# Kernel optimization log

Measured on AMD Instinct MI355X. Metric: run time of the kernel, lower is better.

The kernel has to match this reference:

```python
import jax, jax.numpy as jnp
import numpy as np

LATENT = 32
GRID = 32
G1 = GRID + 1  # 33 samples per axis (align_corners grid)
HID = 128
N_POINTS = 1048576


def _trilinear_sample(emb, points):
    """Faithful F.grid_sample(mode='bilinear', padding_mode='zeros', align_corners=True).
    emb: [(G1)^3, C] flat table; points: [n,3] in [-1,1], (x,y,z) -> (W,H,D)."""
    C = emb.shape[1]
    # torch .view(1, C, D, H, W) on the flat [(G1)^3 * C] buffer: same reshape here.
    vol = emb.reshape(C, G1, G1, G1).transpose(1, 2, 3, 0)  # [D, H, W, C]
    # align_corners=True: u in [-1,1] -> pixel coord (u+1)/2 * (size-1)
    coords = (points + 1.0) * (0.5 * (G1 - 1))
    x, y, z = coords[:, 0], coords[:, 1], coords[:, 2]
    x0 = jnp.floor(x); y0 = jnp.floor(y); z0 = jnp.floor(z)
    fx = x - x0; fy = y - y0; fz = z - z0
    x0i = x0.astype(jnp.int32); y0i = y0.astype(jnp.int32); z0i = z0.astype(jnp.int32)
    x1i = x0i + 1; y1i = y0i + 1; z1i = z0i + 1

    def corner(zi, yi, xi, w):
        valid = ((zi >= 0) & (zi < G1) & (yi >= 0) & (yi < G1)
                 & (xi >= 0) & (xi < G1))
        zc = jnp.clip(zi, 0, G1 - 1)
        yc = jnp.clip(yi, 0, G1 - 1)
        xc = jnp.clip(xi, 0, G1 - 1)
        v = vol[zc, yc, xc]  # [n, C] gather
        return v * (w * valid.astype(w.dtype))[:, None]

    wx0, wx1 = 1.0 - fx, fx
    wy0, wy1 = 1.0 - fy, fy
    wz0, wz1 = 1.0 - fz, fz
    lat = (corner(z0i, y0i, x0i, wz0 * wy0 * wx0)
           + corner(z0i, y0i, x1i, wz0 * wy0 * wx1)
           + corner(z0i, y1i, x0i, wz0 * wy1 * wx0)
           + corner(z0i, y1i, x1i, wz0 * wy1 * wx1)
           + corner(z1i, y0i, x0i, wz1 * wy0 * wx0)
           + corner(z1i, y0i, x1i, wz1 * wy0 * wx1)
           + corner(z1i, y1i, x0i, wz1 * wy1 * wx0)
           + corner(z1i, y1i, x1i, wz1 * wy1 * wx1))
    return lat  # [n, C]


def setup_inputs() -> dict:
    key = jax.random.key(0)
    ks = jax.random.split(key, 8)
    points = jax.random.uniform(ks[0], (N_POINTS, 3), dtype=jnp.float32)  # in [0,1) subset of [-1,1]
    emb = jax.random.normal(ks[1], (G1 ** 3, LATENT), dtype=jnp.float32)
    w1 = jax.random.normal(ks[2], (LATENT, HID), dtype=jnp.float32) * 0.05
    b1 = jax.random.normal(ks[3], (HID,), dtype=jnp.float32) * 0.05
    w2 = jax.random.normal(ks[4], (HID, HID), dtype=jnp.float32) * 0.05
    b2 = jax.random.normal(ks[5], (HID,), dtype=jnp.float32) * 0.05
    w3 = jax.random.normal(ks[6], (HID, 1), dtype=jnp.float32) * 0.05
    b3 = jax.random.normal(ks[7], (1,), dtype=jnp.float32) * 0.05
    return {"points": points, "emb": emb, "w1": w1, "b1": b1,
            "w2": w2, "b2": b2, "w3": w3, "b3": b3}


def reference(points, emb, w1, b1, w2, b2, w3, b3):
    lat = _trilinear_sample(emb, points)                # [n, latent]
    h = jax.nn.relu(lat @ w1 + b1)                      # [n, hid]
    h = jax.nn.relu(h @ w2 + b2)                        # [n, hid]
    sdf = jnp.tanh(h @ w3 + b3)                         # [n, 1]
    return sdf
```

## Files before the change

### kernel.cpp

```cpp
#include <hip/hip_runtime.h>
#include <hip/hip_bf16.h>

#define NPTS 1048576
#define G1I  33
#define NV   35937
#define NC   32
#define HIDD 128

typedef _Float16 h8  __attribute__((ext_vector_type(8)));
typedef _Float16 h4  __attribute__((ext_vector_type(4)));
typedef __fp16   p2  __attribute__((ext_vector_type(2)));
typedef float    f4  __attribute__((ext_vector_type(4)));

#define AS_GLOBAL(p) ((const __attribute__((address_space(1))) char*)(p))
#define AS_LDS(p)    ((__attribute__((address_space(3))) char*)(p))

#define WS_A1  0
#define WS_A2  8192
#define WS_A3  40960
#define WS_EMB 65536
#define WS_NEED (WS_EMB + NV*NC*2)


__global__ __launch_bounds__(256) void vox_prep(
    const float* __restrict__ emb, const float* __restrict__ w1,
    const float* __restrict__ w2, const float* __restrict__ w3,
    char* __restrict__ ws)
{
    __shared__ _Float16 tile[256][NC];
    const int b = blockIdx.x, t = threadIdx.x;
    _Float16* embh = (_Float16*)(ws + WS_EMB);
    if (b < 141) {
        const int v = b*256 + t;
        #pragma unroll
        for (int c = 0; c < NC; ++c) {
            float val = (v < NV) ? emb[c*NV + v] : 0.f;
            const int pos = ((c & 12) << 1) | (c & 3) | ((c >> 4) << 2);
            tile[t][pos] = (_Float16)val;
        }
        __syncthreads();
        if (v < NV) {
            uint4* dst = (uint4*)(embh + v*NC);
            const uint4* src = (const uint4*)&tile[t][0];
            #pragma unroll
            for (int j = 0; j < 4; ++j) dst[j] = src[j];
        }
    } else if (b < 149) {
        const int t2 = b - 141;
        const int ks = t >> 6, l = t & 63;
        const int gq = l >> 4, colh = l & 15;
        _Float16* a2f = (_Float16*)(ws + WS_A2);
        h8 fr;
        #pragma unroll
        for (int i = 0; i < 8; ++i) {
            const int k = 32*ks + 16*(i>>2) + 4*gq + (i&3);
            fr[i] = (_Float16)w2[k*HIDD + 16*t2 + colh];
        }
        *(h8*)(a2f + ((t2*4+ks)*64 + l)*8) = fr;
    } else if (b == 149) {
        _Float16* a1f = (_Float16*)(ws + WS_A1);
        #pragma unroll
        for (int it = 0; it < 2; ++it) {
            const int item = t + it*256;
            const int t8 = item >> 6, l = item & 63;
            const int gq = l >> 4, colh = l & 15;
            h8 fr;
            #pragma unroll
            for (int i = 0; i < 8; ++i) {
                const int k = 16*(i>>2) + 4*gq + (i&3);
                fr[i] = (_Float16)w1[k*HIDD + 16*t8 + colh];
            }
            *(h8*)(a1f + (t8*64 + l)*8) = fr;
        }
    } else {
        _Float16* a3f = (_Float16*)(ws + WS_A3);
        const int j = t >> 6, l = t & 63;
        const int gq = l >> 4;
        h8 fr;
        #pragma unroll
        for (int i = 0; i < 8; ++i) {
            const int k = 32*j + 16*(i>>2) + 4*gq + (i&3);
            fr[i] = (_Float16)w3[k];
        }
        *(h8*)(a3f + (j*64 + l)*8) = fr;
    }
}

__global__ __launch_bounds__(256) void vox_main(
    const float* __restrict__ points, const char* __restrict__ ws,
    const float* __restrict__ b1, const float* __restrict__ b2,
    const float* __restrict__ b3v, float* __restrict__ out)
{
    __shared__ uint4 a2l[2048];

    const int tid  = threadIdx.x;
    const int lane = tid & 63;
    const int wv   = tid >> 6;
    const int gq   = lane >> 4;
    const int colh = lane & 15;

    {
        const uint4* a2g = (const uint4*)(ws + WS_A2);
        #pragma unroll
        for (int j = 0; j < 8; ++j) {
            const uint4* gsrc = a2g + (j*256 + wv*64 + lane);
            uint4*       ldst = ((uint4*)a2l) + (j*256 + wv*64);
            __builtin_amdgcn_global_load_lds(
                (const __attribute__((address_space(1))) void*)AS_GLOBAL(gsrc),
                (__attribute__((address_space(3))) void*)AS_LDS(ldst),
                16, 0, 0);
        }
    }

    const char* embB = (const char*)(ws + WS_EMB);
    const int p = blockIdx.x*256 + tid;
    const float px = points[3*p+0], py = points[3*p+1], pz = points[3*p+2];
    const float xc = (px + 1.f)*16.f, yc = (py + 1.f)*16.f, zc = (pz + 1.f)*16.f;
    const float xf = floorf(xc), yf = floorf(yc), zf = floorf(zc);
    const float fx = xc - xf, fy = yc - yf, fz = zc - zf;
    const int vb = (((int)zf)*G1I + (int)yf)*G1I + (int)xf;

    const h8* a1g = (const h8*)(ws + WS_A1);
    h8 a1fr[8];
    #pragma unroll
    for (int t8 = 0; t8 < 8; ++t8) a1fr[t8] = a1g[t8*64 + lane];

    h8 B2f[4][4];
    #pragma unroll
    for (int pt = 0; pt < 4; ++pt) {
        const int s = pt*16 + colh;
        const float fxs = __shfl(fx, s);
        const float fys = __shfl(fy, s);
        const float fzs = __shfl(fz, s);
        const int   vbs = __shfl(vb, s);
        const char* bz0 = embB + (size_t)((unsigned)vbs*64u + (unsigned)gq*16u);
        const char* bz1 = bz0 + 69696;
        const h8 v0 = *(const h8*)(bz0 +    0);
        const h8 v1 = *(const h8*)(bz0 +   64);
        const h8 v2 = *(const h8*)(bz0 + 2112);
        const h8 v3 = *(const h8*)(bz0 + 2176);
        const h8 v4 = *(const h8*)(bz1 +    0);
        const h8 v5 = *(const h8*)(bz1 +   64);
        const h8 v6 = *(const h8*)(bz1 + 2112);
        const h8 v7 = *(const h8*)(bz1 + 2176);
        const float wx1 = fxs, wx0 = 1.f - fxs;
        const float wy1 = fys, wy0 = 1.f - fys;
        const float wz1 = fzs, wz0 = 1.f - fzs;
        h8 a = (h8){0,0,0,0,0,0,0,0};
        {
            const _Float16 w0 = (_Float16)(wz0*wy0*wx0); const h8 W0 = {w0,w0,w0,w0,w0,w0,w0,w0}; a += W0*v0;
            const _Float16 w1_ = (_Float16)(wz0*wy0*wx1); const h8 W1 = {w1_,w1_,w1_,w1_,w1_,w1_,w1_,w1_}; a += W1*v1;
            const _Float16 w2_ = (_Float16)(wz0*wy1*wx0); const h8 W2 = {w2_,w2_,w2_,w2_,w2_,w2_,w2_,w2_}; a += W2*v2;
            const _Float16 w3_ = (_Float16)(wz0*wy1*wx1); const h8 W3 = {w3_,w3_,w3_,w3_,w3_,w3_,w3_,w3_}; a += W3*v3;
            const _Float16 w4_ = (_Float16)(wz1*wy0*wx0); const h8 W4 = {w4_,w4_,w4_,w4_,w4_,w4_,w4_,w4_}; a += W4*v4;
            const _Float16 w5_ = (_Float16)(wz1*wy0*wx1); const h8 W5 = {w5_,w5_,w5_,w5_,w5_,w5_,w5_,w5_}; a += W5*v5;
            const _Float16 w6_ = (_Float16)(wz1*wy1*wx0); const h8 W6 = {w6_,w6_,w6_,w6_,w6_,w6_,w6_,w6_}; a += W6*v6;
            const _Float16 w7_ = (_Float16)(wz1*wy1*wx1); const h8 W7 = {w7_,w7_,w7_,w7_,w7_,w7_,w7_,w7_}; a += W7*v7;
        }
        f4 acc1[8];
        #pragma unroll
        for (int t8 = 0; t8 < 8; ++t8) acc1[t8] = *(const f4*)(b1 + 16*t8 + 4*gq);
        #pragma unroll
        for (int t8 = 0; t8 < 8; ++t8)
            acc1[t8] = __builtin_amdgcn_mfma_f32_16x16x32_f16(a1fr[t8], a, acc1[t8], 0, 0, 0);
        #pragma unroll
        for (int ks = 0; ks < 4; ++ks) {
            union { h8 v; p2 h[4]; } u;
            const p2 z = {(__fp16)0, (__fp16)0};
            u.h[0] = __builtin_elementwise_max(__builtin_amdgcn_cvt_pkrtz(acc1[2*ks  ][0], acc1[2*ks  ][1]), z);
            u.h[1] = __builtin_elementwise_max(__builtin_amdgcn_cvt_pkrtz(acc1[2*ks  ][2], acc1[2*ks  ][3]), z);
            u.h[2] = __builtin_elementwise_max(__builtin_amdgcn_cvt_pkrtz(acc1[2*ks+1][0], acc1[2*ks+1][1]), z);
            u.h[3] = __builtin_elementwise_max(__builtin_amdgcn_cvt_pkrtz(acc1[2*ks+1][2], acc1[2*ks+1][3]), z);
            B2f[pt][ks] = u.v;
        }
    }

    asm volatile("s_waitcnt vmcnt(0)" ::: "memory");
    __syncthreads();

    const h8* a3g = (const h8*)(ws + WS_A3);
    f4 acc3[4];
    #pragma unroll
    for (int pt = 0; pt < 4; ++pt) acc3[pt] = (f4){0.f,0.f,0.f,0.f};
    #pragma unroll
    for (int q2 = 0; q2 < 4; ++q2) {
        const f4 b2e = *(const f4*)(b2 + 16*(2*q2  ) + 4*gq);
        const f4 b2o = *(const f4*)(b2 + 16*(2*q2+1) + 4*gq);
        f4 acc2e[4], acc2o[4];
        #pragma unroll
        for (int pt = 0; pt < 4; ++pt) { acc2e[pt] = b2e; acc2o[pt] = b2o; }
        #pragma unroll
        for (int ks = 0; ks < 4; ++ks) {
            const h8 fe = *(const h8*)&a2l[((2*q2  )*4 + ks)*64 + lane];
            #pragma unroll
            for (int pt = 0; pt < 4; ++pt)
                acc2e[pt] = __builtin_amdgcn_mfma_f32_16x16x32_f16(fe, B2f[pt][ks], acc2e[pt], 0, 0, 0);
        }
        #pragma unroll
        for (int ks = 0; ks < 4; ++ks) {
            const h8 fo = *(const h8*)&a2l[((2*q2+1)*4 + ks)*64 + lane];
            #pragma unroll
            for (int pt = 0; pt < 4; ++pt)
                acc2o[pt] = __builtin_amdgcn_mfma_f32_16x16x32_f16(fo, B2f[pt][ks], acc2o[pt], 0, 0, 0);
        }
        const h8 a3fr = a3g[q2*64 + lane];
        #pragma unroll
        for (int pt = 0; pt < 4; ++pt) {
            union { h8 v; p2 h[4]; } u;
            const p2 z = {(__fp16)0, (__fp16)0};
            u.h[0] = __builtin_elementwise_max(__builtin_amdgcn_cvt_pkrtz(acc2e[pt][0], acc2e[pt][1]), z);
            u.h[1] = __builtin_elementwise_max(__builtin_amdgcn_cvt_pkrtz(acc2e[pt][2], acc2e[pt][3]), z);
            u.h[2] = __builtin_elementwise_max(__builtin_amdgcn_cvt_pkrtz(acc2o[pt][0], acc2o[pt][1]), z);
            u.h[3] = __builtin_elementwise_max(__builtin_amdgcn_cvt_pkrtz(acc2o[pt][2], acc2o[pt][3]), z);
            acc3[pt] = __builtin_amdgcn_mfma_f32_16x16x32_f16(a3fr, u.v, acc3[pt], 0, 0, 0);
        }
    }

    float sv = 0.f;
    #pragma unroll
    for (int pt = 0; pt < 4; ++pt) if (gq == pt) sv = acc3[pt][0];
    const float zi = sv + b3v[0];
    const float e  = __expf(2.f*zi);
    out[blockIdx.x*256 + tid] = (e - 1.f) / (e + 1.f);
}

extern "C" void kernel_launch(void* const* d_in, const int* in_sizes, int n_in,
                              void* d_out, int out_size, void* d_ws, size_t ws_size,
                              hipStream_t stream)
{
    const float* points = (const float*)d_in[0];
    const float* emb    = (const float*)d_in[1];
    const float* w1     = (const float*)d_in[2];
    const float* b1     = (const float*)d_in[3];
    const float* w2     = (const float*)d_in[4];
    const float* b2     = (const float*)d_in[5];
    const float* w3     = (const float*)d_in[6];
    const float* b3     = (const float*)d_in[7];
    float* out = (float*)d_out;
    char*  ws  = (char*)d_ws;
    if (ws_size < (size_t)WS_NEED) return;

    hipLaunchKernelGGL(vox_prep, dim3(151), dim3(256), 0, stream, emb, w1, w2, w3, ws);
    hipLaunchKernelGGL(vox_main, dim3(NPTS/256), dim3(256), 0, stream,
                       points, ws, b1, b2, b3, out);
}
```

Measured before the change: 144.1 us.

## Gather corner features per 4-lane group then redistribute via ds_bpermute

```diff
diff --git a/kernel.cpp b/kernel.cpp
--- a/kernel.cpp
+++ b/kernel.cpp
@@ -8,7 +8,6 @@
 #define HIDD 128
 
 typedef _Float16 h8  __attribute__((ext_vector_type(8)));
-typedef _Float16 h4  __attribute__((ext_vector_type(4)));
 typedef __fp16   p2  __attribute__((ext_vector_type(2)));
 typedef float    f4  __attribute__((ext_vector_type(4)));
 
@@ -98,6 +97,8 @@
     const int wv   = tid >> 6;
     const int gq   = lane >> 4;
     const int colh = lane & 15;
+    const int q    = lane >> 2;
+    const int ch   = lane & 3;
 
     {
         const uint4* a2g = (const uint4*)(ws + WS_A2);
@@ -113,27 +114,24 @@
     }
 
     const char* embB = (const char*)(ws + WS_EMB);
-    const int p = blockIdx.x*256 + tid;
-    const float px = points[3*p+0], py = points[3*p+1], pz = points[3*p+2];
-    const float xc = (px + 1.f)*16.f, yc = (py + 1.f)*16.f, zc = (pz + 1.f)*16.f;
-    const float xf = floorf(xc), yf = floorf(yc), zf = floorf(zc);
-    const float fx = xc - xf, fy = yc - yf, fz = zc - zf;
-    const int vb = (((int)zf)*G1I + (int)yf)*G1I + (int)xf;
-
-    const h8* a1g = (const h8*)(ws + WS_A1);
-    h8 a1fr[8];
-    #pragma unroll
-    for (int t8 = 0; t8 < 8; ++t8) a1fr[t8] = a1g[t8*64 + lane];
-
-    h8 B2f[4][4];
-    #pragma unroll
-    for (int pt = 0; pt < 4; ++pt) {
-        const int s = pt*16 + colh;
-        const float fxs = __shfl(fx, s);
-        const float fys = __shfl(fy, s);
-        const float fzs = __shfl(fz, s);
-        const int   vbs = __shfl(vb, s);
-        const char* bz0 = embB + (size_t)((unsigned)vbs*64u + (unsigned)gq*16u);
+    const int sgbase = blockIdx.x*256 + wv*64 + q;
+    float px4[4], py4[4], pz4[4];
+    #pragma unroll
+    for (int sh = 0; sh < 4; ++sh) {
+        const float* pp = points + 3*(sgbase + sh*16);
+        px4[sh] = pp[0]; py4[sh] = pp[1]; pz4[sh] = pp[2];
+    }
+
+    h8 accch[4];
+    #pragma unroll
+    for (int sh = 0; sh < 4; ++sh) {
+        const float xc = (px4[sh] + 1.f)*16.f;
+        const float yc = (py4[sh] + 1.f)*16.f;
+        const float zc = (pz4[sh] + 1.f)*16.f;
+        const float xf = floorf(xc), yf = floorf(yc), zf = floorf(zc);
+        const float fxs = xc - xf, fys = yc - yf, fzs = zc - zf;
+        const int vbs = (((int)zf)*G1I + (int)yf)*G1I + (int)xf;
+        const char* bz0 = embB + (size_t)((unsigned)vbs*64u + (unsigned)ch*16u);
         const char* bz1 = bz0 + 69696;
         const h8 v0 = *(const h8*)(bz0 +    0);
         const h8 v1 = *(const h8*)(bz0 +   64);
@@ -147,30 +145,44 @@
         const float wy1 = fys, wy0 = 1.f - fys;
         const float wz1 = fzs, wz0 = 1.f - fzs;
         h8 a = (h8){0,0,0,0,0,0,0,0};
-        {
-            const _Float16 w0 = (_Float16)(wz0*wy0*wx0); const h8 W0 = {w0,w0,w0,w0,w0,w0,w0,w0}; a += W0*v0;
-            const _Float16 w1_ = (_Float16)(wz0*wy0*wx1); const h8 W1 = {w1_,w1_,w1_,w1_,w1_,w1_,w1_,w1_}; a += W1*v1;
-            const _Float16 w2_ = (_Float16)(wz0*wy1*wx0); const h8 W2 = {w2_,w2_,w2_,w2_,w2_,w2_,w2_,w2_}; a += W2*v2;
-            const _Float16 w3_ = (_Float16)(wz0*wy1*wx1); const h8 W3 = {w3_,w3_,w3_,w3_,w3_,w3_,w3_,w3_}; a += W3*v3;
-            const _Float16 w4_ = (_Float16)(wz1*wy0*wx0); const h8 W4 = {w4_,w4_,w4_,w4_,w4_,w4_,w4_,w4_}; a += W4*v4;
-            const _Float16 w5_ = (_Float16)(wz1*wy0*wx1); const h8 W5 = {w5_,w5_,w5_,w5_,w5_,w5_,w5_,w5_}; a += W5*v5;
-            const _Float16 w6_ = (_Float16)(wz1*wy1*wx0); const h8 W6 = {w6_,w6_,w6_,w6_,w6_,w6_,w6_,w6_}; a += W6*v6;
-            const _Float16 w7_ = (_Float16)(wz1*wy1*wx1); const h8 W7 = {w7_,w7_,w7_,w7_,w7_,w7_,w7_,w7_}; a += W7*v7;
-        }
-        f4 acc1[8];
-        #pragma unroll
-        for (int t8 = 0; t8 < 8; ++t8) acc1[t8] = *(const f4*)(b1 + 16*t8 + 4*gq);
-        #pragma unroll
-        for (int t8 = 0; t8 < 8; ++t8)
-            acc1[t8] = __builtin_amdgcn_mfma_f32_16x16x32_f16(a1fr[t8], a, acc1[t8], 0, 0, 0);
+        { const _Float16 w = (_Float16)(wz0*wy0*wx0); const h8 W={w,w,w,w,w,w,w,w}; a += W*v0; }
+        { const _Float16 w = (_Float16)(wz0*wy0*wx1); const h8 W={w,w,w,w,w,w,w,w}; a += W*v1; }
+        { const _Float16 w = (_Float16)(wz0*wy1*wx0); const h8 W={w,w,w,w,w,w,w,w}; a += W*v2; }
+        { const _Float16 w = (_Float16)(wz0*wy1*wx1); const h8 W={w,w,w,w,w,w,w,w}; a += W*v3; }
+        { const _Float16 w = (_Float16)(wz1*wy0*wx0); const h8 W={w,w,w,w,w,w,w,w}; a += W*v4; }
+        { const _Float16 w = (_Float16)(wz1*wy0*wx1); const h8 W={w,w,w,w,w,w,w,w}; a += W*v5; }
+        { const _Float16 w = (_Float16)(wz1*wy1*wx0); const h8 W={w,w,w,w,w,w,w,w}; a += W*v6; }
+        { const _Float16 w = (_Float16)(wz1*wy1*wx1); const h8 W={w,w,w,w,w,w,w,w}; a += W*v7; }
+        accch[sh] = a;
+    }
+
+    const h8* a1g = (const h8*)(ws + WS_A1);
+    h8 a1fr[8];
+    #pragma unroll
+    for (int t8 = 0; t8 < 8; ++t8) a1fr[t8] = a1g[t8*64 + lane];
+
+    const int baddr = 16*colh + 4*gq;
+    h8 B2f[4][4];
+    #pragma unroll
+    for (int pt = 0; pt < 4; ++pt) {
+        union { h8 v; int d[4]; } su, bu;
+        su.v = accch[pt];
+        #pragma unroll
+        for (int j = 0; j < 4; ++j)
+            bu.d[j] = __builtin_amdgcn_ds_bpermute(baddr, su.d[j]);
+        const h8 bf = bu.v;
         #pragma unroll
         for (int ks = 0; ks < 4; ++ks) {
+            f4 ae = *(const f4*)(b1 + 16*(2*ks  ) + 4*gq);
+            f4 ao = *(const f4*)(b1 + 16*(2*ks+1) + 4*gq);
+            ae = __builtin_amdgcn_mfma_f32_16x16x32_f16(a1fr[2*ks  ], bf, ae, 0, 0, 0);
+            ao = __builtin_amdgcn_mfma_f32_16x16x32_f16(a1fr[2*ks+1], bf, ao, 0, 0, 0);
             union { h8 v; p2 h[4]; } u;
             const p2 z = {(__fp16)0, (__fp16)0};
-            u.h[0] = __builtin_elementwise_max(__builtin_amdgcn_cvt_pkrtz(acc1[2*ks  ][0], acc1[2*ks  ][1]), z);
-            u.h[1] = __builtin_elementwise_max(__builtin_amdgcn_cvt_pkrtz(acc1[2*ks  ][2], acc1[2*ks  ][3]), z);
-            u.h[2] = __builtin_elementwise_max(__builtin_amdgcn_cvt_pkrtz(acc1[2*ks+1][0], acc1[2*ks+1][1]), z);
-            u.h[3] = __builtin_elementwise_max(__builtin_amdgcn_cvt_pkrtz(acc1[2*ks+1][2], acc1[2*ks+1][3]), z);
+            u.h[0] = __builtin_elementwise_max(__builtin_amdgcn_cvt_pkrtz(ae[0], ae[1]), z);
+            u.h[1] = __builtin_elementwise_max(__builtin_amdgcn_cvt_pkrtz(ae[2], ae[3]), z);
+            u.h[2] = __builtin_elementwise_max(__builtin_amdgcn_cvt_pkrtz(ao[0], ao[1]), z);
+            u.h[3] = __builtin_elementwise_max(__builtin_amdgcn_cvt_pkrtz(ao[2], ao[3]), z);
             B2f[pt][ks] = u.v;
         }
     }
```

Result: faster. 136.6 us (-5.2%).

## Restructure trilinear gather with software-pipelined loads staged through LDS

Applied to the files above, without the earlier changes.

```diff
diff --git a/kernel.cpp b/kernel.cpp
--- a/kernel.cpp
+++ b/kernel.cpp
@@ -8,7 +8,6 @@
 #define HIDD 128
 
 typedef _Float16 h8  __attribute__((ext_vector_type(8)));
-typedef _Float16 h4  __attribute__((ext_vector_type(4)));
 typedef __fp16   p2  __attribute__((ext_vector_type(2)));
 typedef float    f4  __attribute__((ext_vector_type(4)));
 
@@ -86,18 +85,60 @@
     }
 }
 
+#define G_ISSUE(B, SH)                                                                \
+    float fx##B, fy##B, fz##B;                                                        \
+    h8 B##c0,B##c1,B##c2,B##c3,B##c4,B##c5,B##c6,B##c7;                               \
+    {                                                                                 \
+        const float xc = (px4[SH] + 1.f)*16.f;                                        \
+        const float yc = (py4[SH] + 1.f)*16.f;                                        \
+        const float zc = (pz4[SH] + 1.f)*16.f;                                        \
+        const float xf = floorf(xc), yf = floorf(yc), zf = floorf(zc);                \
+        fx##B = xc - xf; fy##B = yc - yf; fz##B = zc - zf;                            \
+        const int vbs = (((int)zf)*G1I + (int)yf)*G1I + (int)xf;                      \
+        const char* bz0 = embB + (size_t)((unsigned)vbs*64u + (unsigned)ch*16u);      \
+        const char* bz1 = bz0 + 69696;                                                \
+        B##c0 = *(const h8*)(bz0 +    0);                                             \
+        B##c1 = *(const h8*)(bz0 +   64);                                             \
+        B##c2 = *(const h8*)(bz0 + 2112);                                             \
+        B##c3 = *(const h8*)(bz0 + 2176);                                             \
+        B##c4 = *(const h8*)(bz1 +    0);                                             \
+        B##c5 = *(const h8*)(bz1 +   64);                                             \
+        B##c6 = *(const h8*)(bz1 + 2112);                                             \
+        B##c7 = *(const h8*)(bz1 + 2176);                                             \
+    }
+
+#define G_ACCUM(B, SH)                                                                \
+    {                                                                                 \
+        const float wx1 = fx##B, wx0 = 1.f - fx##B;                                   \
+        const float wy1 = fy##B, wy0 = 1.f - fy##B;                                   \
+        const float wz1 = fz##B, wz0 = 1.f - fz##B;                                   \
+        h8 a = (h8){0,0,0,0,0,0,0,0};                                                 \
+        { const _Float16 w = (_Float16)(wz0*wy0*wx0); const h8 W={w,w,w,w,w,w,w,w}; a += W*B##c0; } \
+        { const _Float16 w = (_Float16)(wz0*wy0*wx1); const h8 W={w,w,w,w,w,w,w,w}; a += W*B##c1; } \
+        { const _Float16 w = (_Float16)(wz0*wy1*wx0); const h8 W={w,w,w,w,w,w,w,w}; a += W*B##c2; } \
+        { const _Float16 w = (_Float16)(wz0*wy1*wx1); const h8 W={w,w,w,w,w,w,w,w}; a += W*B##c3; } \
+        { const _Float16 w = (_Float16)(wz1*wy0*wx0); const h8 W={w,w,w,w,w,w,w,w}; a += W*B##c4; } \
+        { const _Float16 w = (_Float16)(wz1*wy0*wx1); const h8 W={w,w,w,w,w,w,w,w}; a += W*B##c5; } \
+        { const _Float16 w = (_Float16)(wz1*wy1*wx0); const h8 W={w,w,w,w,w,w,w,w}; a += W*B##c6; } \
+        { const _Float16 w = (_Float16)(wz1*wy1*wx1); const h8 W={w,w,w,w,w,w,w,w}; a += W*B##c7; } \
+        *(uint4*)&latl[wv*64 + (SH)*16 + q][8*ch] = *(uint4*)&a;                      \
+    }
+
 __global__ __launch_bounds__(256) void vox_main(
     const float* __restrict__ points, const char* __restrict__ ws,
     const float* __restrict__ b1, const float* __restrict__ b2,
     const float* __restrict__ b3v, float* __restrict__ out)
 {
-    __shared__ uint4 a2l[2048];
+    __shared__ _Float16 latl[256][40];
+    __shared__ uint4    a2l[2048];
 
     const int tid  = threadIdx.x;
     const int lane = tid & 63;
     const int wv   = tid >> 6;
     const int gq   = lane >> 4;
     const int colh = lane & 15;
+    const int q    = lane >> 2;
+    const int ch   = lane & 3;
 
     {
         const uint4* a2g = (const uint4*)(ws + WS_A2);
@@ -113,12 +154,23 @@
     }
 
     const char* embB = (const char*)(ws + WS_EMB);
-    const int p = blockIdx.x*256 + tid;
-    const float px = points[3*p+0], py = points[3*p+1], pz = points[3*p+2];
-    const float xc = (px + 1.f)*16.f, yc = (py + 1.f)*16.f, zc = (pz + 1.f)*16.f;
-    const float xf = floorf(xc), yf = floorf(yc), zf = floorf(zc);
-    const float fx = xc - xf, fy = yc - yf, fz = zc - zf;
-    const int vb = (((int)zf)*G1I + (int)yf)*G1I + (int)xf;
+    const int sgbase = blockIdx.x*256 + wv*64 + q;
+    float px4[4], py4[4], pz4[4];
+    #pragma unroll
+    for (int sh = 0; sh < 4; ++sh) {
+        const float* pp = points + 3*(sgbase + sh*16);
+        px4[sh] = pp[0]; py4[sh] = pp[1]; pz4[sh] = pp[2];
+    }
+
+    G_ISSUE(GA, 0)
+    G_ISSUE(GB, 1)
+    G_ACCUM(GA, 0)
+    G_ISSUE(GC, 2)
+    G_ACCUM(GB, 1)
+    G_ISSUE(GD, 3)
+    G_ACCUM(GC, 2)
+    G_ACCUM(GD, 3)
+    asm volatile("s_waitcnt lgkmcnt(0)" ::: "memory");
 
     const h8* a1g = (const h8*)(ws + WS_A1);
     h8 a1fr[8];
@@ -128,41 +180,15 @@
     h8 B2f[4][4];
     #pragma unroll
     for (int pt = 0; pt < 4; ++pt) {
-        const int s = pt*16 + colh;
-        const float fxs = __shfl(fx, s);
-        const float fys = __shfl(fy, s);
-        const float fzs = __shfl(fz, s);
-        const int   vbs = __shfl(vb, s);
-        const char* bz0 = embB + (size_t)((unsigned)vbs*64u + (unsigned)gq*16u);
-        const char* bz1 = bz0 + 69696;
-        const h8 v0 = *(const h8*)(bz0 +    0);
-        const h8 v1 = *(const h8*)(bz0 +   64);
-        const h8 v2 = *(const h8*)(bz0 + 2112);
-        const h8 v3 = *(const h8*)(bz0 + 2176);
-        const h8 v4 = *(const h8*)(bz1 +    0);
-        const h8 v5 = *(const h8*)(bz1 +   64);
-        const h8 v6 = *(const h8*)(bz1 + 2112);
-        const h8 v7 = *(const h8*)(bz1 + 2176);
-        const float wx1 = fxs, wx0 = 1.f - fxs;
-        const float wy1 = fys, wy0 = 1.f - fys;
-        const float wz1 = fzs, wz0 = 1.f - fzs;
-        h8 a = (h8){0,0,0,0,0,0,0,0};
-        {
-            const _Float16 w0 = (_Float16)(wz0*wy0*wx0); const h8 W0 = {w0,w0,w0,w0,w0,w0,w0,w0}; a += W0*v0;
-            const _Float16 w1_ = (_Float16)(wz0*wy0*wx1); const h8 W1 = {w1_,w1_,w1_,w1_,w1_,w1_,w1_,w1_}; a += W1*v1;
-            const _Float16 w2_ = (_Float16)(wz0*wy1*wx0); const h8 W2 = {w2_,w2_,w2_,w2_,w2_,w2_,w2_,w2_}; a += W2*v2;
-            const _Float16 w3_ = (_Float16)(wz0*wy1*wx1); const h8 W3 = {w3_,w3_,w3_,w3_,w3_,w3_,w3_,w3_}; a += W3*v3;
-            const _Float16 w4_ = (_Float16)(wz1*wy0*wx0); const h8 W4 = {w4_,w4_,w4_,w4_,w4_,w4_,w4_,w4_}; a += W4*v4;
-            const _Float16 w5_ = (_Float16)(wz1*wy0*wx1); const h8 W5 = {w5_,w5_,w5_,w5_,w5_,w5_,w5_,w5_}; a += W5*v5;
-            const _Float16 w6_ = (_Float16)(wz1*wy1*wx0); const h8 W6 = {w6_,w6_,w6_,w6_,w6_,w6_,w6_,w6_}; a += W6*v6;
-            const _Float16 w7_ = (_Float16)(wz1*wy1*wx1); const h8 W7 = {w7_,w7_,w7_,w7_,w7_,w7_,w7_,w7_}; a += W7*v7;
-        }
+        const h8 bf = *(const h8*)&latl[wv*64 + pt*16 + colh][8*gq];
         f4 acc1[8];
         #pragma unroll
         for (int t8 = 0; t8 < 8; ++t8) acc1[t8] = *(const f4*)(b1 + 16*t8 + 4*gq);
+        __builtin_amdgcn_s_setprio(1);
         #pragma unroll
         for (int t8 = 0; t8 < 8; ++t8)
-            acc1[t8] = __builtin_amdgcn_mfma_f32_16x16x32_f16(a1fr[t8], a, acc1[t8], 0, 0, 0);
+            acc1[t8] = __builtin_amdgcn_mfma_f32_16x16x32_f16(a1fr[t8], bf, acc1[t8], 0, 0, 0);
+        __builtin_amdgcn_s_setprio(0);
         #pragma unroll
         for (int ks = 0; ks < 4; ++ks) {
             union { h8 v; p2 h[4]; } u;
@@ -189,6 +215,7 @@
         f4 acc2e[4], acc2o[4];
         #pragma unroll
         for (int pt = 0; pt < 4; ++pt) { acc2e[pt] = b2e; acc2o[pt] = b2o; }
+        __builtin_amdgcn_s_setprio(1);
         #pragma unroll
         for (int ks = 0; ks < 4; ++ks) {
             const h8 fe = *(const h8*)&a2l[((2*q2  )*4 + ks)*64 + lane];
@@ -203,6 +230,7 @@
             for (int pt = 0; pt < 4; ++pt)
                 acc2o[pt] = __builtin_amdgcn_mfma_f32_16x16x32_f16(fo, B2f[pt][ks], acc2o[pt], 0, 0, 0);
         }
+        __builtin_amdgcn_s_setprio(0);
         const h8 a3fr = a3g[q2*64 + lane];
         #pragma unroll
         for (int pt = 0; pt < 4; ++pt) {
```

Measured after the change: 140.1 us. 2.7% less time.
